# Kernel tuning notes

Measured on AMD Instinct MI355X. Metric: run time of the kernel, lower is better.

Reference implementation:

```python
import jax, jax.numpy as jnp
import numpy as np

N = 10000      # nodes
E = 160000     # edges
F_IN = 128     # input_dim
HID = 128      # hidden_dim = per-head channels (concat=False)
OUT = 128      # output_dim
H = 4          # heads
L = 4          # layers (all 128->128 here, so params stack)


def setup_inputs() -> dict:
    key = jax.random.key(0)
    ks = jax.random.split(key, 12)
    x = jax.random.normal(ks[0], (N, F_IN), dtype=jnp.float32)
    edge_index = jax.random.randint(ks[1], (2, E), 0, N, dtype=jnp.int64)
    s = 1.0 / np.sqrt(F_IN)
    Wq = jax.random.normal(ks[2], (L, F_IN, H * HID), dtype=jnp.float32) * s
    bq = jnp.zeros((L, H * HID), dtype=jnp.float32)
    Wk = jax.random.normal(ks[3], (L, F_IN, H * HID), dtype=jnp.float32) * s
    bk = jnp.zeros((L, H * HID), dtype=jnp.float32)
    Wv = jax.random.normal(ks[4], (L, F_IN, H * HID), dtype=jnp.float32) * s
    bv = jnp.zeros((L, H * HID), dtype=jnp.float32)
    Wskip = jax.random.normal(ks[5], (L, F_IN, HID), dtype=jnp.float32) * s
    bskip = jnp.zeros((L, HID), dtype=jnp.float32)
    return {"x": x, "edge_index": edge_index, "Wq": Wq, "bq": bq,
            "Wk": Wk, "bk": bk, "Wv": Wv, "bv": bv,
            "Wskip": Wskip, "bskip": bskip}


def _transformer_conv(x, src, dst, Wq, bq, Wk, bk, Wv, bv, Ws, bs):
    # PyG TransformerConv, concat=False (mean over heads), root_weight=True
    n = x.shape[0]
    q = (x @ Wq + bq).reshape(n, H, HID)
    k = (x @ Wk + bk).reshape(n, H, HID)
    v = (x @ Wv + bv).reshape(n, H, HID)
    # per-edge attention logits: [E, H]
    alpha = jnp.einsum('ehc,ehc->eh', q[dst], k[src]) / jnp.sqrt(jnp.float32(HID))
    # segment softmax over destination node
    m = jax.ops.segment_max(alpha, dst, num_segments=n)          # [N, H]
    e = jnp.exp(alpha - m[dst])                                  # [E, H]
    z = jax.ops.segment_sum(e, dst, num_segments=n)              # [N, H]
    a = e / z[dst]                                               # [E, H]
    msg = a[:, :, None] * v[src]                                 # [E, H, C]
    out = jax.ops.segment_sum(msg, dst, num_segments=n)          # [N, H, C]
    out = out.mean(axis=1)                                       # concat=False
    return out + x @ Ws + bs                                     # skip (root_weight)


def reference(x, edge_index, Wq, bq, Wk, bk, Wv, bv, Wskip, bskip):
    src = edge_index[0]
    dst = edge_index[1]
    h = x
    for l in range(L - 1):
        h = _transformer_conv(h, src, dst, Wq[l], bq[l], Wk[l], bk[l],
                              Wv[l], bv[l], Wskip[l], bskip[l])
        h = jax.nn.relu(h)  # dropout p in eval/reference is identity
    h = _transformer_conv(h, src, dst, Wq[-1], bq[-1], Wk[-1], bk[-1],
                          Wv[-1], bv[-1], Wskip[-1], bskip[-1])
    return h
```

## Files before the change

### kernel.cpp

```cpp
#include <hip/hip_runtime.h>
#include <math.h>

static constexpr int F  = 128;
static constexpr int H  = 4;
static constexpr int HF = 512;
static constexpr int NCP = 640;
static constexpr int LAYERS = 4;

typedef __attribute__((ext_vector_type(8))) short bf16x8;
typedef __attribute__((ext_vector_type(4))) float f32x4;

__device__ __forceinline__ unsigned short f2bf(float f) {
    union { float f; unsigned u; } v; v.f = f;
    unsigned r = (v.u + 0x7FFFu + ((v.u >> 16) & 1u)) >> 16;
    return (unsigned short)r;
}
__device__ __forceinline__ float bf2f(unsigned short b) {
    union { unsigned u; float f; } v; v.u = ((unsigned)b) << 16;
    return v.f;
}

__device__ __forceinline__ float row16_sum(float x) {
    int t;
    t = __builtin_amdgcn_update_dpp(0, __float_as_int(x), 0xB1, 0xF, 0xF, true);
    x += __int_as_float(t);
    t = __builtin_amdgcn_update_dpp(0, __float_as_int(x), 0x4E, 0xF, 0xF, true);
    x += __int_as_float(t);
    t = __builtin_amdgcn_update_dpp(0, __float_as_int(x), 0x124, 0xF, 0xF, true);
    x += __int_as_float(t);
    t = __builtin_amdgcn_update_dpp(0, __float_as_int(x), 0x128, 0xF, 0xF, true);
    x += __int_as_float(t);
    return x;
}

__global__ void hist_kernel(const int* __restrict__ dst, int* __restrict__ deg, int E) {
    int e = blockIdx.x * blockDim.x + threadIdx.x;
    if (e < E) atomicAdd(&deg[dst[e]], 1);
}

__global__ void scan_kernel(const int* __restrict__ deg, int* __restrict__ row_ptr, int n) {
    __shared__ int wsum[16];
    __shared__ int carry_s, wtot_s;
    const int tid = threadIdx.x;
    const int lane = tid & 63;
    const int wid = tid >> 6;
    if (tid == 0) { carry_s = 0; row_ptr[0] = 0; }
    __syncthreads();
    for (int base = 0; base < n; base += 1024) {
        int i = base + tid;
        int x = (i < n) ? deg[i] : 0;
#pragma unroll
        for (int off = 1; off < 64; off <<= 1) {
            int t = __shfl_up(x, off, 64);
            if (lane >= off) x += t;
        }
        if (lane == 63) wsum[wid] = x;
        __syncthreads();
        if (tid == 0) {
            int s = 0;
#pragma unroll
            for (int j = 0; j < 16; ++j) { int t = wsum[j]; wsum[j] = s; s += t; }
            wtot_s = s;
        }
        __syncthreads();
        int incl = x + wsum[wid] + carry_s;
        if (i < n) row_ptr[i + 1] = incl;
        __syncthreads();
        if (tid == 0) carry_s += wtot_s;
        __syncthreads();
    }
}

__global__ void scatter_kernel(const int* __restrict__ src, const int* __restrict__ dst,
                               const int* __restrict__ row_ptr, int* __restrict__ cursor,
                               int* __restrict__ csr_src, int E) {
    int e = blockIdx.x * blockDim.x + threadIdx.x;
    if (e < E) {
        int d = dst[e];
        int pos = atomicAdd(&cursor[d], 1);
        csr_src[row_ptr[d] + pos] = src[e];
    }
}

static constexpr int NB_CONV  = 1250;
static constexpr int NB_WQK   = 64;
static constexpr int NB_WS    = 64;
static constexpr int NB_BPOST = 256;
static constexpr int NB_BIAS  = LAYERS;
static constexpr int NB_PREP  = NB_CONV + NB_WQK + NB_WS + NB_BPOST + NB_BIAS;

__global__ __launch_bounds__(256) void prep_kernel(
    const float* __restrict__ x, unsigned short* __restrict__ h_bf, int n4,
    const float* __restrict__ Wq, const float* __restrict__ Wk,
    const float* __restrict__ Wv, const float* __restrict__ Ws,
    const float* __restrict__ bq, const float* __restrict__ bs, const float* __restrict__ bv,
    unsigned short* __restrict__ Bpre, unsigned short* __restrict__ Bpost,
    float* __restrict__ biasPre, float* __restrict__ biasPost, float scale)
{
    __shared__ __attribute__((aligned(16))) float smem[64 * 33 * 2];
    const int tid = threadIdx.x;
    int b = blockIdx.x;

    if (b < NB_CONV) {
        int i = b * 256 + tid;
        if (i < n4) {
            float4 v = *(const float4*)(x + (size_t)i * 4);
            ushort4 o;
            o.x = f2bf(v.x); o.y = f2bf(v.y); o.z = f2bf(v.z); o.w = f2bf(v.w);
            *(ushort4*)(h_bf + (size_t)i * 4) = o;
        }
        return;
    }
    b -= NB_CONV;
    if (b < NB_WQK) {
        float (*As)[33] = (float (*)[33])smem;
        float (*Bs)[33] = (float (*)[33])(smem + 64 * 33);
        const int bx = b & 1, by = (b >> 1) & 1, lh = b >> 2;
        const int l = lh >> 2, h = lh & 3;
        const int c0 = by * 64, k0 = bx * 64;
        const float* Ab = Wk + (size_t)l * 65536 + h * 128;
        const float* Bb = Wq + (size_t)l * 65536 + h * 128;
        const int tx = tid & 15, ty = tid >> 4;
        float acc[4][4] = {};
        for (int jj = 0; jj < 128; jj += 32) {
#pragma unroll
            for (int rep = 0; rep < 2; ++rep) {
                int f = tid + rep * 256;
                int r = f >> 3, j4 = (f & 7) * 4;
                float4 a = *(const float4*)(Ab + (size_t)(c0 + r) * 512 + jj + j4);
                As[r][j4 + 0] = a.x; As[r][j4 + 1] = a.y; As[r][j4 + 2] = a.z; As[r][j4 + 3] = a.w;
                float4 bb = *(const float4*)(Bb + (size_t)(k0 + r) * 512 + jj + j4);
                Bs[r][j4 + 0] = bb.x; Bs[r][j4 + 1] = bb.y; Bs[r][j4 + 2] = bb.z; Bs[r][j4 + 3] = bb.w;
            }
            __syncthreads();
#pragma unroll
            for (int j = 0; j < 32; ++j) {
                float a0 = As[ty * 4 + 0][j], a1 = As[ty * 4 + 1][j];
                float a2 = As[ty * 4 + 2][j], a3 = As[ty * 4 + 3][j];
                float b0 = Bs[tx * 4 + 0][j], b1 = Bs[tx * 4 + 1][j];
                float b2 = Bs[tx * 4 + 2][j], b3 = Bs[tx * 4 + 3][j];
                acc[0][0] += a0 * b0; acc[0][1] += a0 * b1; acc[0][2] += a0 * b2; acc[0][3] += a0 * b3;
                acc[1][0] += a1 * b0; acc[1][1] += a1 * b1; acc[1][2] += a1 * b2; acc[1][3] += a1 * b3;
                acc[2][0] += a2 * b0; acc[2][1] += a2 * b1; acc[2][2] += a2 * b2; acc[2][3] += a2 * b3;
                acc[3][0] += a3 * b0; acc[3][1] += a3 * b1; acc[3][2] += a3 * b2; acc[3][3] += a3 * b3;
            }
            __syncthreads();
        }
#pragma unroll
        for (int i = 0; i < 4; ++i)
#pragma unroll
            for (int t = 0; t < 4; ++t) {
                int c = c0 + ty * 4 + i;
                int k = k0 + tx * 4 + t;
                Bpre[(size_t)l * NCP * 128 + (size_t)(h * 128 + c) * 128 + k] = f2bf(scale * acc[i][t]);
            }
        return;
    }
    b -= NB_WQK;
    if (b < NB_WS) {
        unsigned short (*t)[33] = (unsigned short (*)[33])smem;
        const int bx = b & 3, by = (b >> 2) & 3, l = b >> 4;
        const int k0 = bx * 32, n0 = by * 32;
        const int cx = tid & 31, ry = tid >> 5;
#pragma unroll
        for (int rr = 0; rr < 32; rr += 8) {
            int k = k0 + ry + rr;
            t[ry + rr][cx] = f2bf(Ws[(size_t)l * 16384 + (size_t)k * 128 + n0 + cx]);
        }
        __syncthreads();
#pragma unroll
        for (int rr = 0; rr < 32; rr += 8) {
            int n = n0 + ry + rr;
            Bpre[(size_t)l * NCP * 128 + (size_t)(512 + n) * 128 + k0 + cx] = t[cx][ry + rr];
        }
        return;
    }
    b -= NB_WS;
    if (b < NB_BPOST) {
        unsigned short (*t)[33] = (unsigned short (*)[33])smem;
        const int bx = b & 3, by = (b >> 2) & 3, lh = b >> 4;
        const int l = lh >> 2, h = lh & 3;
        const int ci0 = bx * 32, co0 = by * 32;
        const int cx = tid & 31, ry = tid >> 5;
#pragma unroll
        for (int rr = 0; rr < 32; rr += 8) {
            int ci = ci0 + ry + rr;
            t[ry + rr][cx] = f2bf(0.25f * Wv[(size_t)l * 65536 + (size_t)ci * 512 + h * 128 + co0 + cx]);
        }
        __syncthreads();
#pragma unroll
        for (int rr = 0; rr < 32; rr += 8) {
            int co = co0 + ry + rr;
            Bpost[(size_t)l * 65536 + (size_t)co * 512 + h * 128 + ci0 + cx] = t[cx][ry + rr];
        }
        return;
    }
    b -= NB_BPOST;
    {
        const int l = b;
        for (int n = tid; n < 512; n += 256) {
            int h = n >> 7, c = n & 127;
            float s = 0.f;
            for (int j = 0; j < 128; ++j)
                s += bq[(size_t)l * 512 + h * 128 + j] * Wk[(size_t)l * 65536 + (size_t)c * 512 + h * 128 + j];
            biasPre[(size_t)l * NCP + n] = s * scale;
        }
        for (int c = tid; c < 128; c += 256) {
            float s = 0.f;
            for (int h = 0; h < 4; ++h) s += bv[(size_t)l * 512 + h * 128 + c];
            biasPost[(size_t)l * 128 + c] = 0.25f * s + bs[(size_t)l * 128 + c];
        }
    }
}

__global__ __launch_bounds__(256) void gemm_pre(
    const unsigned short* __restrict__ Abf,
    const unsigned short* __restrict__ Bt,
    const float* __restrict__ bias,
    unsigned short* __restrict__ Qt,
    int M)
{
    __shared__ unsigned short As[128][72];
    __shared__ unsigned short Bs[128][72];

    const int tid = threadIdx.x;
    const int wave = tid >> 6, lane = tid & 63;
    const int lane16 = lane & 15, quad = lane >> 4;
    const int wr = wave >> 1, wc = wave & 1;
    const int row0 = blockIdx.y * 128;
    const int col0 = blockIdx.x * 128;

    f32x4 acc[4][4] = {};

    for (int kk = 0; kk < 128; kk += 64) {
#pragma unroll
        for (int j = 0; j < 4; ++j) {
            int c = tid + j * 256;
            int r = c >> 3, c8 = (c & 7) * 8;
            bf16x8 v = {};
            if (row0 + r < M) v = *(const bf16x8*)(Abf + (size_t)(row0 + r) * 128 + kk + c8);
            *(bf16x8*)&As[r][c8] = v;
        }
#pragma unroll
        for (int j = 0; j < 4; ++j) {
            int c = tid + j * 256;
            int r = c >> 3, c8 = (c & 7) * 8;
            *(bf16x8*)&Bs[r][c8] = *(const bf16x8*)(Bt + (size_t)(col0 + r) * 128 + kk + c8);
        }
        __syncthreads();

#pragma unroll
        for (int ks = 0; ks < 2; ++ks) {
            bf16x8 a[4], b[4];
#pragma unroll
            for (int i = 0; i < 4; ++i)
                a[i] = *(const bf16x8*)&As[wr * 64 + i * 16 + lane16][ks * 32 + quad * 8];
#pragma unroll
            for (int i = 0; i < 4; ++i)
                b[i] = *(const bf16x8*)&Bs[wc * 64 + i * 16 + lane16][ks * 32 + quad * 8];
#pragma unroll
            for (int mi = 0; mi < 4; ++mi)
#pragma unroll
                for (int ni = 0; ni < 4; ++ni)
                    acc[mi][ni] = __builtin_amdgcn_mfma_f32_16x16x32_bf16(
                        a[mi], b[ni], acc[mi][ni], 0, 0, 0);
        }
        __syncthreads();
    }

#pragma unroll
    for (int mi = 0; mi < 4; ++mi) {
        int rowb = row0 + wr * 64 + mi * 16 + quad * 4;
#pragma unroll
        for (int ni = 0; ni < 4; ++ni) {
            int col = col0 + wc * 64 + ni * 16 + lane16;
            float bv = bias[col];
#pragma unroll
            for (int r = 0; r < 4; ++r) {
                int gr = rowb + r;
                if (gr < M) Qt[(size_t)gr * 512 + col] = f2bf(acc[mi][ni][r] + bv);
            }
        }
    }
}

__global__ __launch_bounds__(128, 4) void attn_agg(
    const unsigned short* __restrict__ Qt,
    const unsigned short* __restrict__ Hb,
    const int* __restrict__ row_ptr,
    const int* __restrict__ csr_src,
    unsigned short* __restrict__ Agg,
    int N)
{
    __shared__ float part[4][16][10];

    const int tid = threadIdx.x;
    const int wv  = tid >> 6;
    const int g   = (tid >> 4) & 3;
    const int l16 = tid & 15;
    const int node = blockIdx.x;

    const float NEG = -3e38f;

    float qf[8];
    {
        bf16x8 qv = *(const bf16x8*)(Qt + (size_t)node * HF + g * F + l16 * 8);
#pragma unroll
        for (int j = 0; j < 8; ++j) qf[j] = bf2f((unsigned short)qv[j]);
    }
    const unsigned short* Hl = Hb + (size_t)l16 * 8;

    const int beg = row_ptr[node];
    const int end = row_ptr[node + 1];

    float m = NEG, z = 0.f;
    float acc[8];
#pragma unroll
    for (int j = 0; j < 8; ++j) acc[j] = 0.f;

    const int begw = beg + wv * 4;
    if (begw < end) {
        const int last = end - 1;
        const int NB = (end - begw + 7) >> 3;

#define CLD(i) csr_src[(i) < last ? (i) : last]

        int a0 = CLD(begw + 0), a1 = CLD(begw + 1), a2 = CLD(begw + 2), a3 = CLD(begw + 3);
        bf16x8 hA0 = *(const bf16x8*)(Hl + (size_t)a0 * F);
        bf16x8 hA1 = *(const bf16x8*)(Hl + (size_t)a1 * F);
        bf16x8 hA2 = *(const bf16x8*)(Hl + (size_t)a2 * F);
        bf16x8 hA3 = *(const bf16x8*)(Hl + (size_t)a3 * F);
        int b0 = CLD(begw + 8), b1 = CLD(begw + 9), b2 = CLD(begw + 10), b3 = CLD(begw + 11);
        bf16x8 hB0 = *(const bf16x8*)(Hl + (size_t)b0 * F);
        bf16x8 hB1 = *(const bf16x8*)(Hl + (size_t)b1 * F);
        bf16x8 hB2 = *(const bf16x8*)(Hl + (size_t)b2 * F);
        bf16x8 hB3 = *(const bf16x8*)(Hl + (size_t)b3 * F);
        a0 = CLD(begw + 16); a1 = CLD(begw + 17); a2 = CLD(begw + 18); a3 = CLD(begw + 19);
        b0 = CLD(begw + 24); b1 = CLD(begw + 25); b2 = CLD(begw + 26); b3 = CLD(begw + 27);
        __builtin_amdgcn_sched_barrier(0);

#define ATTN_BATCH(H0, H1, H2, H3, I0, I1, I2, I3)                              \
    {                                                                           \
        float hf[4][8];                                                         \
        _Pragma("unroll")                                                       \
        for (int j = 0; j < 8; ++j) {                                           \
            hf[0][j] = bf2f((unsigned short)H0[j]);                             \
            hf[1][j] = bf2f((unsigned short)H1[j]);                             \
            hf[2][j] = bf2f((unsigned short)H2[j]);                             \
            hf[3][j] = bf2f((unsigned short)H3[j]);                             \
        }                                                                       \
        if (k + 2 < NB) {                                                       \
            H0 = *(const bf16x8*)(Hl + (size_t)I0 * F);                         \
            H1 = *(const bf16x8*)(Hl + (size_t)I1 * F);                         \
            H2 = *(const bf16x8*)(Hl + (size_t)I2 * F);                         \
            H3 = *(const bf16x8*)(Hl + (size_t)I3 * F);                         \
            I0 = CLD(base + 32); I1 = CLD(base + 33);                           \
            I2 = CLD(base + 34); I3 = CLD(base + 35);                           \
        }                                                                       \
        __builtin_amdgcn_sched_barrier(0);   \
        float p0 = 0.f, p1 = 0.f, p2 = 0.f, p3 = 0.f;                           \
        _Pragma("unroll")                                                       \
        for (int j = 0; j < 8; ++j) {                                           \
            p0 += qf[j] * hf[0][j]; p1 += qf[j] * hf[1][j];                     \
            p2 += qf[j] * hf[2][j]; p3 += qf[j] * hf[3][j];                     \
        }                                                                       \
        p0 = row16_sum(p0); p1 = row16_sum(p1);                                 \
        p2 = row16_sum(p2); p3 = row16_sum(p3);                                 \
        const int nv = end - base;                                              \
        if (nv < 4) { if (nv < 2) p1 = NEG; if (nv < 3) p2 = NEG; p3 = NEG; }   \
        float bm = fmaxf(fmaxf(p0, p1), fmaxf(p2, p3));                         \
        float mn = fmaxf(m, bm);                                                \
        float rs = exp2f(m - mn);                                               \
        float w0 = exp2f(p0 - mn), w1 = exp2f(p1 - mn);                         \
        float w2 = exp2f(p2 - mn), w3 = exp2f(p3 - mn);                         \
        z = z * rs + (w0 + w1) + (w2 + w3);                                     \
        _Pragma("unroll")                                                       \
        for (int j = 0; j < 8; ++j)                                             \
            acc[j] = acc[j] * rs + w0 * hf[0][j] + w1 * hf[1][j]                \
                   + w2 * hf[2][j] + w3 * hf[3][j];                             \
        m = mn;                                                                 \
    }

        int base = begw;
        int k = 0;
        for (;;) {
            ATTN_BATCH(hA0, hA1, hA2, hA3, a0, a1, a2, a3)
            ++k; base += 8;
            if (k >= NB) break;
            ATTN_BATCH(hB0, hB1, hB2, hB3, b0, b1, b2, b3)
            ++k; base += 8;
            if (k >= NB) break;
        }
#undef ATTN_BATCH
#undef CLD
    }

    if (wv == 1) {
#pragma unroll
        for (int j = 0; j < 8; ++j) part[g][l16][j] = acc[j];
        part[g][l16][8] = m;
        part[g][l16][9] = z;
    }
    __syncthreads();
    if (wv == 0) {
        float om = part[g][l16][8];
        float oz = part[g][l16][9];
        float M  = fmaxf(m, om);
        float sa = exp2f(m - M);
        float sb = exp2f(om - M);
        float zz = z * sa + oz * sb;
        float inv = (zz > 0.f) ? 1.f / zz : 0.f;
        bf16x8 o;
#pragma unroll
        for (int j = 0; j < 8; ++j)
            o[j] = (short)f2bf((acc[j] * sa + part[g][l16][j] * sb) * inv);
        *(bf16x8*)(Agg + (size_t)node * HF + g * F + l16 * 8) = o;
    }
}

__global__ __launch_bounds__(256) void gemm_post(
    const unsigned short* __restrict__ Agg,
    const unsigned short* __restrict__ Hc,
    const unsigned short* __restrict__ Bt,
    const unsigned short* __restrict__ Bsk,
    const float* __restrict__ bias,
    float* __restrict__ out_f,
    unsigned short* __restrict__ out_bf,
    int relu, int M)
{
    __shared__ unsigned short As[64][72];
    __shared__ unsigned short Bs[64][72];

    const int tid = threadIdx.x;
    const int wave = tid >> 6, lane = tid & 63;
    const int lane16 = lane & 15, quad = lane >> 4;
    const int row0 = blockIdx.y * 64;
    const int col0 = blockIdx.x * 64;

    f32x4 acc[4] = {};

    for (int kk = 0; kk < 640; kk += 64) {
        const bool sk = kk >= 512;
        const int k0 = sk ? kk - 512 : kk;
#pragma unroll
        for (int rep = 0; rep < 2; ++rep) {
            int c = tid + rep * 256;
            int r = c >> 3, c8 = (c & 7) * 8;
            bf16x8 v = {};
            if (row0 + r < M)
                v = sk ? *(const bf16x8*)(Hc  + (size_t)(row0 + r) * 128 + k0 + c8)
                       : *(const bf16x8*)(Agg + (size_t)(row0 + r) * 512 + k0 + c8);
            *(bf16x8*)&As[r][c8] = v;
            *(bf16x8*)&Bs[r][c8] = sk
                ? *(const bf16x8*)(Bsk + (size_t)(col0 + r) * 128 + k0 + c8)
                : *(const bf16x8*)(Bt  + (size_t)(col0 + r) * 512 + k0 + c8);
        }
        __syncthreads();

#pragma unroll
        for (int ks = 0; ks < 2; ++ks) {
            bf16x8 b = *(const bf16x8*)&Bs[wave * 16 + lane16][ks * 32 + quad * 8];
#pragma unroll
            for (int mt = 0; mt < 4; ++mt) {
                bf16x8 a = *(const bf16x8*)&As[mt * 16 + lane16][ks * 32 + quad * 8];
                acc[mt] = __builtin_amdgcn_mfma_f32_16x16x32_bf16(a, b, acc[mt], 0, 0, 0);
            }
        }
        __syncthreads();
    }

    const int col = col0 + wave * 16 + lane16;
    const float bcol = bias[col];
#pragma unroll
    for (int mt = 0; mt < 4; ++mt) {
#pragma unroll
        for (int r = 0; r < 4; ++r) {
            int row = row0 + mt * 16 + quad * 4 + r;
            if (row < M) {
                float v = acc[mt][r] + bcol;
                if (relu) v = fmaxf(v, 0.f);
                if (out_f)  out_f[(size_t)row * 128 + col] = v;
                if (out_bf) out_bf[(size_t)row * 128 + col] = f2bf(v);
            }
        }
    }
}

extern "C" void kernel_launch(void* const* d_in, const int* in_sizes, int n_in,
                              void* d_out, int out_size, void* d_ws, size_t ws_size,
                              hipStream_t stream) {
    const float* x     = (const float*)d_in[0];
    const int*   ei    = (const int*)d_in[1];
    const float* Wq    = (const float*)d_in[2];
    const float* bq    = (const float*)d_in[3];
    const float* Wk    = (const float*)d_in[4];
    const float* bk    = (const float*)d_in[5];
    const float* Wv    = (const float*)d_in[6];
    const float* bv    = (const float*)d_in[7];
    const float* Wskip = (const float*)d_in[8];
    const float* bskip = (const float*)d_in[9];
    float* out = (float*)d_out;
    (void)bk;

    const int N = in_sizes[0] / F;
    const int E = in_sizes[1] / 2;
    const float scale = 0.08838834764831845f * 1.4426950408889634f;

    const int* src = ei;
    const int* dst = ei + E;

    char* p = (char*)d_ws;
    float* biasPreP = (float*)p;               p += (size_t)LAYERS * NCP * sizeof(float);
    float* biasPostP= (float*)p;               p += (size_t)LAYERS * 128 * sizeof(float);
    unsigned short* h0    = (unsigned short*)p; p += (size_t)N * F * sizeof(unsigned short);
    unsigned short* h1    = (unsigned short*)p; p += (size_t)N * F * sizeof(unsigned short);
    unsigned short* Qt    = (unsigned short*)p; p += (size_t)N * HF * sizeof(unsigned short);
    unsigned short* AggB  = (unsigned short*)p; p += (size_t)N * HF * sizeof(unsigned short);
    unsigned short* BpreP = (unsigned short*)p; p += (size_t)LAYERS * NCP * 128 * sizeof(unsigned short);
    unsigned short* BpostP= (unsigned short*)p; p += (size_t)LAYERS * 128 * 512 * sizeof(unsigned short);
    int* deg     = (int*)p;                    p += (size_t)N * sizeof(int);
    int* cursor  = (int*)p;                    p += (size_t)N * sizeof(int);
    int* row_ptr = (int*)p;                    p += (size_t)(N + 1) * sizeof(int);
    int* csr_src = (int*)p;

    hipMemsetAsync(deg, 0, 2 * (size_t)N * sizeof(int), stream);
    {
        int blocks = (E + 255) / 256;
        hist_kernel<<<blocks, 256, 0, stream>>>(dst, deg, E);
        scan_kernel<<<1, 1024, 0, stream>>>(deg, row_ptr, N);
        scatter_kernel<<<blocks, 256, 0, stream>>>(src, dst, row_ptr, cursor, csr_src, E);
    }

    prep_kernel<<<NB_PREP, 256, 0, stream>>>(x, h0, N * F / 4,
                                             Wq, Wk, Wv, Wskip,
                                             bq, bskip, bv,
                                             BpreP, BpostP, biasPreP, biasPostP, scale);

    const int rowBlocks128 = (N + 127) / 128;
    const int rowBlocks64  = (N + 63) / 64;

    unsigned short* hcur = h0;
    unsigned short* hnxt = h1;
    for (int l = 0; l < LAYERS; ++l) {
        dim3 gridPre(4, rowBlocks128);
        gemm_pre<<<gridPre, 256, 0, stream>>>(hcur,
                                              BpreP + (size_t)l * NCP * 128,
                                              biasPreP + (size_t)l * NCP,
                                              Qt, N);

        attn_agg<<<N, 128, 0, stream>>>(Qt, hcur, row_ptr, csr_src, AggB, N);

        float* out_f = nullptr;
        unsigned short* out_bf = nullptr;
        int relu;
        if (l == LAYERS - 1) { out_f = out; relu = 0; }
        else { out_bf = hnxt; relu = 1; }

        dim3 gridPost(2, rowBlocks64);
        gemm_post<<<gridPost, 256, 0, stream>>>(AggB, hcur,
                                                BpostP + (size_t)l * 128 * 512,
                                                BpreP + (size_t)l * NCP * 128 + (size_t)512 * 128,
                                                biasPostP + (size_t)l * 128,
                                                out_f, out_bf, relu, N);

        unsigned short* t = hcur; hcur = hnxt; hnxt = t;
    }
}
```

Measured before the change: 254.1 us.

## Fuse all layer stages into one persistent cooperative kernel with grid syncs

```diff
diff --git a/kernel.cpp b/kernel.cpp
--- a/kernel.cpp
+++ b/kernel.cpp
@@ -1,5 +1,8 @@
 #include <hip/hip_runtime.h>
+#include <hip/hip_cooperative_groups.h>
 #include <math.h>
+
+namespace cg = cooperative_groups;
 
 static constexpr int F  = 128;
 static constexpr int H  = 4;
@@ -213,131 +216,137 @@
     }
 }
 
-__global__ __launch_bounds__(256) void gemm_pre(
-    const unsigned short* __restrict__ Abf,
-    const unsigned short* __restrict__ Bt,
-    const float* __restrict__ bias,
-    unsigned short* __restrict__ Qt,
-    int M)
+__global__ __launch_bounds__(256) void layers_kernel(
+    unsigned short* __restrict__ h0, unsigned short* __restrict__ h1,
+    unsigned short* __restrict__ Qt, unsigned short* __restrict__ Agg,
+    const unsigned short* __restrict__ Bpre, const unsigned short* __restrict__ Bpost,
+    const float* __restrict__ biasPre, const float* __restrict__ biasPost,
+    const int* __restrict__ row_ptr, const int* __restrict__ csr_src,
+    float* __restrict__ out, int N)
 {
-    __shared__ unsigned short As[128][72];
-    __shared__ unsigned short Bs[128][72];
+    cg::grid_group grid = cg::this_grid();
+    __shared__ __attribute__((aligned(16))) char smem[36864];
 
     const int tid = threadIdx.x;
-    const int wave = tid >> 6, lane = tid & 63;
-    const int lane16 = lane & 15, quad = lane >> 4;
-    const int wr = wave >> 1, wc = wave & 1;
-    const int row0 = blockIdx.y * 128;
-    const int col0 = blockIdx.x * 128;
-
-    f32x4 acc[4][4] = {};
-
-    for (int kk = 0; kk < 128; kk += 64) {
-#pragma unroll
-        for (int j = 0; j < 4; ++j) {
-            int c = tid + j * 256;
-            int r = c >> 3, c8 = (c & 7) * 8;
-            bf16x8 v = {};
-            if (row0 + r < M) v = *(const bf16x8*)(Abf + (size_t)(row0 + r) * 128 + kk + c8);
-            *(bf16x8*)&As[r][c8] = v;
-        }
-#pragma unroll
-        for (int j = 0; j < 4; ++j) {
-            int c = tid + j * 256;
-            int r = c >> 3, c8 = (c & 7) * 8;
-            *(bf16x8*)&Bs[r][c8] = *(const bf16x8*)(Bt + (size_t)(col0 + r) * 128 + kk + c8);
-        }
-        __syncthreads();
-
-#pragma unroll
-        for (int ks = 0; ks < 2; ++ks) {
-            bf16x8 a[4], b[4];
-#pragma unroll
-            for (int i = 0; i < 4; ++i)
-                a[i] = *(const bf16x8*)&As[wr * 64 + i * 16 + lane16][ks * 32 + quad * 8];
-#pragma unroll
-            for (int i = 0; i < 4; ++i)
-                b[i] = *(const bf16x8*)&Bs[wc * 64 + i * 16 + lane16][ks * 32 + quad * 8];
-#pragma unroll
-            for (int mi = 0; mi < 4; ++mi)
-#pragma unroll
-                for (int ni = 0; ni < 4; ++ni)
-                    acc[mi][ni] = __builtin_amdgcn_mfma_f32_16x16x32_bf16(
-                        a[mi], b[ni], acc[mi][ni], 0, 0, 0);
-        }
-        __syncthreads();
-    }
-
-#pragma unroll
-    for (int mi = 0; mi < 4; ++mi) {
-        int rowb = row0 + wr * 64 + mi * 16 + quad * 4;
-#pragma unroll
-        for (int ni = 0; ni < 4; ++ni) {
-            int col = col0 + wc * 64 + ni * 16 + lane16;
-            float bv = bias[col];
-#pragma unroll
-            for (int r = 0; r < 4; ++r) {
-                int gr = rowb + r;
-                if (gr < M) Qt[(size_t)gr * 512 + col] = f2bf(acc[mi][ni][r] + bv);
+    const int rb128 = (N + 127) >> 7;
+    const int rb64  = (N + 63) >> 6;
+    const float NEG = -3e38f;
+
+    unsigned short* hcur = h0;
+    unsigned short* hnxt = h1;
+
+    for (int l = 0; l < LAYERS; ++l) {
+        const unsigned short* BtPre = Bpre + (size_t)l * NCP * 128;
+        const float* bPre = biasPre + (size_t)l * NCP;
+
+        {
+            unsigned short (*As)[72] = (unsigned short (*)[72])smem;
+            unsigned short (*Bs)[72] = (unsigned short (*)[72])(smem + 128 * 72 * 2);
+            const int wave = tid >> 6, lane = tid & 63;
+            const int lane16 = lane & 15, quad = lane >> 4;
+            const int wr = wave >> 1, wc = wave & 1;
+            const int nT = 4 * rb128;
+            for (int tile = blockIdx.x; tile < nT; tile += gridDim.x) {
+                const int row0 = (tile >> 2) * 128;
+                const int col0 = (tile & 3) * 128;
+                f32x4 acc[4][4] = {};
+                for (int kk = 0; kk < 128; kk += 64) {
+#pragma unroll
+                    for (int j = 0; j < 4; ++j) {
+                        int c = tid + j * 256;
+                        int r = c >> 3, c8 = (c & 7) * 8;
+                        bf16x8 v = {};
+                        if (row0 + r < N) v = *(const bf16x8*)(hcur + (size_t)(row0 + r) * 128 + kk + c8);
+                        *(bf16x8*)&As[r][c8] = v;
+                    }
+#pragma unroll
+                    for (int j = 0; j < 4; ++j) {
+                        int c = tid + j * 256;
+                        int r = c >> 3, c8 = (c & 7) * 8;
+                        *(bf16x8*)&Bs[r][c8] = *(const bf16x8*)(BtPre + (size_t)(col0 + r) * 128 + kk + c8);
+                    }
+                    __syncthreads();
+#pragma unroll
+                    for (int ks = 0; ks < 2; ++ks) {
+                        bf16x8 a[4], b[4];
+#pragma unroll
+                        for (int i = 0; i < 4; ++i)
+                            a[i] = *(const bf16x8*)&As[wr * 64 + i * 16 + lane16][ks * 32 + quad * 8];
+#pragma unroll
+                        for (int i = 0; i < 4; ++i)
+                            b[i] = *(const bf16x8*)&Bs[wc * 64 + i * 16 + lane16][ks * 32 + quad * 8];
+#pragma unroll
+                        for (int mi = 0; mi < 4; ++mi)
+#pragma unroll
+                            for (int ni = 0; ni < 4; ++ni)
+                                acc[mi][ni] = __builtin_amdgcn_mfma_f32_16x16x32_bf16(
+                                    a[mi], b[ni], acc[mi][ni], 0, 0, 0);
+                    }
+                    __syncthreads();
+                }
+#pragma unroll
+                for (int mi = 0; mi < 4; ++mi) {
+                    int rowb = row0 + wr * 64 + mi * 16 + quad * 4;
+#pragma unroll
+                    for (int ni = 0; ni < 4; ++ni) {
+                        int col = col0 + wc * 64 + ni * 16 + lane16;
+                        float bv = bPre[col];
+#pragma unroll
+                        for (int r = 0; r < 4; ++r) {
+                            int gr = rowb + r;
+                            if (gr < N) Qt[(size_t)gr * 512 + col] = f2bf(acc[mi][ni][r] + bv);
+                        }
+                    }
+                }
             }
         }
-    }
-}
-
-__global__ __launch_bounds__(128, 4) void attn_agg(
-    const unsigned short* __restrict__ Qt,
-    const unsigned short* __restrict__ Hb,
-    const int* __restrict__ row_ptr,
-    const int* __restrict__ csr_src,
-    unsigned short* __restrict__ Agg,
-    int N)
-{
-    __shared__ float part[4][16][10];
-
-    const int tid = threadIdx.x;
-    const int wv  = tid >> 6;
-    const int g   = (tid >> 4) & 3;
-    const int l16 = tid & 15;
-    const int node = blockIdx.x;
-
-    const float NEG = -3e38f;
-
-    float qf[8];
-    {
-        bf16x8 qv = *(const bf16x8*)(Qt + (size_t)node * HF + g * F + l16 * 8);
-#pragma unroll
-        for (int j = 0; j < 8; ++j) qf[j] = bf2f((unsigned short)qv[j]);
-    }
-    const unsigned short* Hl = Hb + (size_t)l16 * 8;
-
-    const int beg = row_ptr[node];
-    const int end = row_ptr[node + 1];
-
-    float m = NEG, z = 0.f;
-    float acc[8];
-#pragma unroll
-    for (int j = 0; j < 8; ++j) acc[j] = 0.f;
-
-    const int begw = beg + wv * 4;
-    if (begw < end) {
-        const int last = end - 1;
-        const int NB = (end - begw + 7) >> 3;
+        grid.sync();
+
+        {
+            float (*part)[16][10] = (float (*)[16][10])smem;
+            const int half = tid >> 7;
+            const int wv  = (tid >> 6) & 1;
+            const int g   = (tid >> 4) & 3;
+            const int l16 = tid & 15;
+            const unsigned short* Hl = hcur + (size_t)l16 * 8;
+
+            for (int nb = blockIdx.x * 2; nb < N; nb += gridDim.x * 2) {
+                const int node = nb + half;
+                const bool valid = node < N;
+
+                float m = NEG, z = 0.f;
+                float acc[8];
+#pragma unroll
+                for (int j = 0; j < 8; ++j) acc[j] = 0.f;
+
+                if (valid) {
+                    float qf[8];
+                    {
+                        bf16x8 qv = *(const bf16x8*)(Qt + (size_t)node * HF + g * F + l16 * 8);
+#pragma unroll
+                        for (int j = 0; j < 8; ++j) qf[j] = bf2f((unsigned short)qv[j]);
+                    }
+                    const int beg = row_ptr[node];
+                    const int end = row_ptr[node + 1];
+                    const int begw = beg + wv * 4;
+                    if (begw < end) {
+                        const int last = end - 1;
+                        const int NB = (end - begw + 7) >> 3;
 
 #define CLD(i) csr_src[(i) < last ? (i) : last]
-
-        int a0 = CLD(begw + 0), a1 = CLD(begw + 1), a2 = CLD(begw + 2), a3 = CLD(begw + 3);
-        bf16x8 hA0 = *(const bf16x8*)(Hl + (size_t)a0 * F);
-        bf16x8 hA1 = *(const bf16x8*)(Hl + (size_t)a1 * F);
-        bf16x8 hA2 = *(const bf16x8*)(Hl + (size_t)a2 * F);
-        bf16x8 hA3 = *(const bf16x8*)(Hl + (size_t)a3 * F);
-        int b0 = CLD(begw + 8), b1 = CLD(begw + 9), b2 = CLD(begw + 10), b3 = CLD(begw + 11);
-        bf16x8 hB0 = *(const bf16x8*)(Hl + (size_t)b0 * F);
-        bf16x8 hB1 = *(const bf16x8*)(Hl + (size_t)b1 * F);
-        bf16x8 hB2 = *(const bf16x8*)(Hl + (size_t)b2 * F);
-        bf16x8 hB3 = *(const bf16x8*)(Hl + (size_t)b3 * F);
-        a0 = CLD(begw + 16); a1 = CLD(begw + 17); a2 = CLD(begw + 18); a3 = CLD(begw + 19);
-        b0 = CLD(begw + 24); b1 = CLD(begw + 25); b2 = CLD(begw + 26); b3 = CLD(begw + 27);
-        __builtin_amdgcn_sched_barrier(0);
+                        int a0 = CLD(begw + 0), a1 = CLD(begw + 1), a2 = CLD(begw + 2), a3 = CLD(begw + 3);
+                        bf16x8 hA0 = *(const bf16x8*)(Hl + (size_t)a0 * F);
+                        bf16x8 hA1 = *(const bf16x8*)(Hl + (size_t)a1 * F);
+                        bf16x8 hA2 = *(const bf16x8*)(Hl + (size_t)a2 * F);
+                        bf16x8 hA3 = *(const bf16x8*)(Hl + (size_t)a3 * F);
+                        int b0 = CLD(begw + 8), b1 = CLD(begw + 9), b2 = CLD(begw + 10), b3 = CLD(begw + 11);
+                        bf16x8 hB0 = *(const bf16x8*)(Hl + (size_t)b0 * F);
+                        bf16x8 hB1 = *(const bf16x8*)(Hl + (size_t)b1 * F);
+                        bf16x8 hB2 = *(const bf16x8*)(Hl + (size_t)b2 * F);
+                        bf16x8 hB3 = *(const bf16x8*)(Hl + (size_t)b3 * F);
+                        a0 = CLD(begw + 16); a1 = CLD(begw + 17); a2 = CLD(begw + 18); a3 = CLD(begw + 19);
+                        b0 = CLD(begw + 24); b1 = CLD(begw + 25); b2 = CLD(begw + 26); b3 = CLD(begw + 27);
+                        __builtin_amdgcn_sched_barrier(0);
 
 #define ATTN_BATCH(H0, H1, H2, H3, I0, I1, I2, I3)                              \
     {                                                                           \
@@ -357,7 +366,7 @@
             I0 = CLD(base + 32); I1 = CLD(base + 33);                           \
             I2 = CLD(base + 34); I3 = CLD(base + 35);                           \
         }                                                                       \
-        __builtin_amdgcn_sched_barrier(0);   \
+        __builtin_amdgcn_sched_barrier(0);                                      \
         float p0 = 0.f, p1 = 0.f, p2 = 0.f, p3 = 0.f;                           \
         _Pragma("unroll")                                                       \
         for (int j = 0; j < 8; ++j) {                                           \
@@ -381,6 +390,262 @@
         m = mn;                                                                 \
     }
 
+                        int base = begw;
+                        int k = 0;
+                        for (;;) {
+                            ATTN_BATCH(hA0, hA1, hA2, hA3, a0, a1, a2, a3)
+                            ++k; base += 8;
+                            if (k >= NB) break;
+                            ATTN_BATCH(hB0, hB1, hB2, hB3, b0, b1, b2, b3)
+                            ++k; base += 8;
+                            if (k >= NB) break;
+                        }
+#undef ATTN_BATCH
+#undef CLD
+                    }
+                }
+                __syncthreads();
+                if (valid && wv == 1) {
+#pragma unroll
+                    for (int j = 0; j < 8; ++j) part[(half << 2) + g][l16][j] = acc[j];
+                    part[(half << 2) + g][l16][8] = m;
+                    part[(half << 2) + g][l16][9] = z;
+                }
+                __syncthreads();
+                if (valid && wv == 0) {
+                    float om = part[(half << 2) + g][l16][8];
+                    float oz = part[(half << 2) + g][l16][9];
+                    float M  = fmaxf(m, om);
+                    float sa = exp2f(m - M);
+                    float sb = exp2f(om - M);
+                    float zz = z * sa + oz * sb;
+                    float inv = (zz > 0.f) ? 1.f / zz : 0.f;
+                    bf16x8 o;
+#pragma unroll
+                    for (int j = 0; j < 8; ++j)
+                        o[j] = (short)f2bf((acc[j] * sa + part[(half << 2) + g][l16][j] * sb) * inv);
+                    *(bf16x8*)(Agg + (size_t)node * HF + g * F + l16 * 8) = o;
+                }
+                __syncthreads();
+            }
+        }
+        grid.sync();
+
+        {
+            const unsigned short* BtPost = Bpost + (size_t)l * 128 * 512;
+            const unsigned short* Bsk = Bpre + (size_t)l * NCP * 128 + (size_t)512 * 128;
+            const float* bPost = biasPost + (size_t)l * 128;
+            float* out_f = (l == LAYERS - 1) ? out : nullptr;
+            unsigned short* out_bf = (l == LAYERS - 1) ? nullptr : hnxt;
+            const int relu = (l == LAYERS - 1) ? 0 : 1;
+
+            unsigned short (*As)[72] = (unsigned short (*)[72])smem;
+            unsigned short (*Bs)[72] = (unsigned short (*)[72])(smem + 64 * 72 * 2);
+            const int wave = tid >> 6, lane = tid & 63;
+            const int lane16 = lane & 15, quad = lane >> 4;
+            const int nT = 2 * rb64;
+            for (int tile = blockIdx.x; tile < nT; tile += gridDim.x) {
+                const int row0 = (tile >> 1) * 64;
+                const int col0 = (tile & 1) * 64;
+                f32x4 acc[4] = {};
+                for (int kk = 0; kk < 640; kk += 64) {
+                    const bool sk = kk >= 512;
+                    const int k0 = sk ? kk - 512 : kk;
+#pragma unroll
+                    for (int rep = 0; rep < 2; ++rep) {
+                        int c = tid + rep * 256;
+                        int r = c >> 3, c8 = (c & 7) * 8;
+                        bf16x8 v = {};
+                        if (row0 + r < N)
+                            v = sk ? *(const bf16x8*)(hcur + (size_t)(row0 + r) * 128 + k0 + c8)
+                                   : *(const bf16x8*)(Agg  + (size_t)(row0 + r) * 512 + k0 + c8);
+                        *(bf16x8*)&As[r][c8] = v;
+                        *(bf16x8*)&Bs[r][c8] = sk
+                            ? *(const bf16x8*)(Bsk    + (size_t)(col0 + r) * 128 + k0 + c8)
+                            : *(const bf16x8*)(BtPost + (size_t)(col0 + r) * 512 + k0 + c8);
+                    }
+                    __syncthreads();
+#pragma unroll
+                    for (int ks = 0; ks < 2; ++ks) {
+                        bf16x8 b = *(const bf16x8*)&Bs[wave * 16 + lane16][ks * 32 + quad * 8];
+#pragma unroll
+                        for (int mt = 0; mt < 4; ++mt) {
+                            bf16x8 a = *(const bf16x8*)&As[mt * 16 + lane16][ks * 32 + quad * 8];
+                            acc[mt] = __builtin_amdgcn_mfma_f32_16x16x32_bf16(a, b, acc[mt], 0, 0, 0);
+                        }
+                    }
+                    __syncthreads();
+                }
+                const int col = col0 + wave * 16 + lane16;
+                const float bcol = bPost[col];
+#pragma unroll
+                for (int mt = 0; mt < 4; ++mt) {
+#pragma unroll
+                    for (int r = 0; r < 4; ++r) {
+                        int row = row0 + mt * 16 + quad * 4 + r;
+                        if (row < N) {
+                            float v = acc[mt][r] + bcol;
+                            if (relu) v = fmaxf(v, 0.f);
+                            if (out_f)  out_f[(size_t)row * 128 + col] = v;
+                            if (out_bf) out_bf[(size_t)row * 128 + col] = f2bf(v);
+                        }
+                    }
+                }
+            }
+        }
+        grid.sync();
+
+        unsigned short* t = hcur; hcur = hnxt; hnxt = t;
+    }
+}
+
+__global__ __launch_bounds__(256) void gemm_pre(
+    const unsigned short* __restrict__ Abf, const unsigned short* __restrict__ Bt,
+    const float* __restrict__ bias, unsigned short* __restrict__ Qt, int M)
+{
+    __shared__ unsigned short As[128][72];
+    __shared__ unsigned short Bs[128][72];
+    const int tid = threadIdx.x;
+    const int wave = tid >> 6, lane = tid & 63;
+    const int lane16 = lane & 15, quad = lane >> 4;
+    const int wr = wave >> 1, wc = wave & 1;
+    const int row0 = blockIdx.y * 128;
+    const int col0 = blockIdx.x * 128;
+    f32x4 acc[4][4] = {};
+    for (int kk = 0; kk < 128; kk += 64) {
+#pragma unroll
+        for (int j = 0; j < 4; ++j) {
+            int c = tid + j * 256;
+            int r = c >> 3, c8 = (c & 7) * 8;
+            bf16x8 v = {};
+            if (row0 + r < M) v = *(const bf16x8*)(Abf + (size_t)(row0 + r) * 128 + kk + c8);
+            *(bf16x8*)&As[r][c8] = v;
+        }
+#pragma unroll
+        for (int j = 0; j < 4; ++j) {
+            int c = tid + j * 256;
+            int r = c >> 3, c8 = (c & 7) * 8;
+            *(bf16x8*)&Bs[r][c8] = *(const bf16x8*)(Bt + (size_t)(col0 + r) * 128 + kk + c8);
+        }
+        __syncthreads();
+#pragma unroll
+        for (int ks = 0; ks < 2; ++ks) {
+            bf16x8 a[4], b[4];
+#pragma unroll
+            for (int i = 0; i < 4; ++i)
+                a[i] = *(const bf16x8*)&As[wr * 64 + i * 16 + lane16][ks * 32 + quad * 8];
+#pragma unroll
+            for (int i = 0; i < 4; ++i)
+                b[i] = *(const bf16x8*)&Bs[wc * 64 + i * 16 + lane16][ks * 32 + quad * 8];
+#pragma unroll
+            for (int mi = 0; mi < 4; ++mi)
+#pragma unroll
+                for (int ni = 0; ni < 4; ++ni)
+                    acc[mi][ni] = __builtin_amdgcn_mfma_f32_16x16x32_bf16(
+                        a[mi], b[ni], acc[mi][ni], 0, 0, 0);
+        }
+        __syncthreads();
+    }
+#pragma unroll
+    for (int mi = 0; mi < 4; ++mi) {
+        int rowb = row0 + wr * 64 + mi * 16 + quad * 4;
+#pragma unroll
+        for (int ni = 0; ni < 4; ++ni) {
+            int col = col0 + wc * 64 + ni * 16 + lane16;
+            float bv = bias[col];
+#pragma unroll
+            for (int r = 0; r < 4; ++r) {
+                int gr = rowb + r;
+                if (gr < M) Qt[(size_t)gr * 512 + col] = f2bf(acc[mi][ni][r] + bv);
+            }
+        }
+    }
+}
+
+__global__ __launch_bounds__(128, 4) void attn_agg(
+    const unsigned short* __restrict__ Qt, const unsigned short* __restrict__ Hb,
+    const int* __restrict__ row_ptr, const int* __restrict__ csr_src,
+    unsigned short* __restrict__ Agg, int N)
+{
+    __shared__ float part[4][16][10];
+    const int tid = threadIdx.x;
+    const int wv  = tid >> 6;
+    const int g   = (tid >> 4) & 3;
+    const int l16 = tid & 15;
+    const int node = blockIdx.x;
+    const float NEG = -3e38f;
+    float qf[8];
+    {
+        bf16x8 qv = *(const bf16x8*)(Qt + (size_t)node * HF + g * F + l16 * 8);
+#pragma unroll
+        for (int j = 0; j < 8; ++j) qf[j] = bf2f((unsigned short)qv[j]);
+    }
+    const unsigned short* Hl = Hb + (size_t)l16 * 8;
+    const int beg = row_ptr[node];
+    const int end = row_ptr[node + 1];
+    float m = NEG, z = 0.f;
+    float acc[8];
+#pragma unroll
+    for (int j = 0; j < 8; ++j) acc[j] = 0.f;
+    const int begw = beg + wv * 4;
+    if (begw < end) {
+        const int last = end - 1;
+        const int NB = (end - begw + 7) >> 3;
+#define CLD(i) csr_src[(i) < last ? (i) : last]
+        int a0 = CLD(begw + 0), a1 = CLD(begw + 1), a2 = CLD(begw + 2), a3 = CLD(begw + 3);
+        bf16x8 hA0 = *(const bf16x8*)(Hl + (size_t)a0 * F);
+        bf16x8 hA1 = *(const bf16x8*)(Hl + (size_t)a1 * F);
+        bf16x8 hA2 = *(const bf16x8*)(Hl + (size_t)a2 * F);
+        bf16x8 hA3 = *(const bf16x8*)(Hl + (size_t)a3 * F);
+        int b0 = CLD(begw + 8), b1 = CLD(begw + 9), b2 = CLD(begw + 10), b3 = CLD(begw + 11);
+        bf16x8 hB0 = *(const bf16x8*)(Hl + (size_t)b0 * F);
+        bf16x8 hB1 = *(const bf16x8*)(Hl + (size_t)b1 * F);
+        bf16x8 hB2 = *(const bf16x8*)(Hl + (size_t)b2 * F);
+        bf16x8 hB3 = *(const bf16x8*)(Hl + (size_t)b3 * F);
+        a0 = CLD(begw + 16); a1 = CLD(begw + 17); a2 = CLD(begw + 18); a3 = CLD(begw + 19);
+        b0 = CLD(begw + 24); b1 = CLD(begw + 25); b2 = CLD(begw + 26); b3 = CLD(begw + 27);
+        __builtin_amdgcn_sched_barrier(0);
+#define ATTN_BATCH(H0, H1, H2, H3, I0, I1, I2, I3)                              \
+    {                                                                           \
+        float hf[4][8];                                                         \
+        _Pragma("unroll")                                                       \
+        for (int j = 0; j < 8; ++j) {                                           \
+            hf[0][j] = bf2f((unsigned short)H0[j]);                             \
+            hf[1][j] = bf2f((unsigned short)H1[j]);                             \
+            hf[2][j] = bf2f((unsigned short)H2[j]);                             \
+            hf[3][j] = bf2f((unsigned short)H3[j]);                             \
+        }                                                                       \
+        if (k + 2 < NB) {                                                       \
+            H0 = *(const bf16x8*)(Hl + (size_t)I0 * F);                         \
+            H1 = *(const bf16x8*)(Hl + (size_t)I1 * F);                         \
+            H2 = *(const bf16x8*)(Hl + (size_t)I2 * F);                         \
+            H3 = *(const bf16x8*)(Hl + (size_t)I3 * F);                         \
+            I0 = CLD(base + 32); I1 = CLD(base + 33);                           \
+            I2 = CLD(base + 34); I3 = CLD(base + 35);                           \
+        }                                                                       \
+        __builtin_amdgcn_sched_barrier(0);                                      \
+        float p0 = 0.f, p1 = 0.f, p2 = 0.f, p3 = 0.f;                           \
+        _Pragma("unroll")                                                       \
+        for (int j = 0; j < 8; ++j) {                                           \
+            p0 += qf[j] * hf[0][j]; p1 += qf[j] * hf[1][j];                     \
+            p2 += qf[j] * hf[2][j]; p3 += qf[j] * hf[3][j];                     \
+        }                                                                       \
+        p0 = row16_sum(p0); p1 = row16_sum(p1);                                 \
+        p2 = row16_sum(p2); p3 = row16_sum(p3);                                 \
+        const int nv = end - base;                                              \
+        if (nv < 4) { if (nv < 2) p1 = NEG; if (nv < 3) p2 = NEG; p3 = NEG; }   \
+        float bm = fmaxf(fmaxf(p0, p1), fmaxf(p2, p3));                         \
+        float mn = fmaxf(m, bm);                                                \
+        float rs = exp2f(m - mn);                                               \
+        float w0 = exp2f(p0 - mn), w1 = exp2f(p1 - mn);                         \
+        float w2 = exp2f(p2 - mn), w3 = exp2f(p3 - mn);                         \
+        z = z * rs + (w0 + w1) + (w2 + w3);                                     \
+        _Pragma("unroll")                                                       \
+        for (int j = 0; j < 8; ++j)                                             \
+            acc[j] = acc[j] * rs + w0 * hf[0][j] + w1 * hf[1][j]                \
+                   + w2 * hf[2][j] + w3 * hf[3][j];                             \
+        m = mn;                                                                 \
+    }
         int base = begw;
         int k = 0;
         for (;;) {
@@ -394,7 +659,6 @@
 #undef ATTN_BATCH
 #undef CLD
     }
-
     if (wv == 1) {
 #pragma unroll
         for (int j = 0; j < 8; ++j) part[g][l16][j] = acc[j];
@@ -419,26 +683,19 @@
 }
 
 __global__ __launch_bounds__(256) void gemm_post(
-    const unsigned short* __restrict__ Agg,
-    const unsigned short* __restrict__ Hc,
-    const unsigned short* __restrict__ Bt,
-    const unsigned short* __restrict__ Bsk,
-    const float* __restrict__ bias,
-    float* __restrict__ out_f,
-    unsigned short* __restrict__ out_bf,
-    int relu, int M)
+    const unsigned short* __restrict__ Agg, const unsigned short* __restrict__ Hc,
+    const unsigned short* __restrict__ Bt, const unsigned short* __restrict__ Bsk,
+    const float* __restrict__ bias, float* __restrict__ out_f,
+    unsigned short* __restrict__ out_bf, int relu, int M)
 {
     __shared__ unsigned short As[64][72];
     __shared__ unsigned short Bs[64][72];
-
     const int tid = threadIdx.x;
     const int wave = tid >> 6, lane = tid & 63;
     const int lane16 = lane & 15, quad = lane >> 4;
     const int row0 = blockIdx.y * 64;
     const int col0 = blockIdx.x * 64;
-
     f32x4 acc[4] = {};
-
     for (int kk = 0; kk < 640; kk += 64) {
         const bool sk = kk >= 512;
         const int k0 = sk ? kk - 512 : kk;
@@ -456,7 +713,6 @@
                 : *(const bf16x8*)(Bt  + (size_t)(col0 + r) * 512 + k0 + c8);
         }
         __syncthreads();
-
 #pragma unroll
         for (int ks = 0; ks < 2; ++ks) {
             bf16x8 b = *(const bf16x8*)&Bs[wave * 16 + lane16][ks * 32 + quad * 8];
@@ -468,7 +724,6 @@
         }
         __syncthreads();
     }
-
     const int col = col0 + wave * 16 + lane16;
     const float bcol = bias[col];
 #pragma unroll
@@ -536,33 +791,49 @@
                                              bq, bskip, bv,
                                              BpreP, BpostP, biasPreP, biasPostP, scale);
 
-    const int rowBlocks128 = (N + 127) / 128;
-    const int rowBlocks64  = (N + 63) / 64;
-
-    unsigned short* hcur = h0;
-    unsigned short* hnxt = h1;
-    for (int l = 0; l < LAYERS; ++l) {
-        dim3 gridPre(4, rowBlocks128);
-        gemm_pre<<<gridPre, 256, 0, stream>>>(hcur,
-                                              BpreP + (size_t)l * NCP * 128,
-                                              biasPreP + (size_t)l * NCP,
-                                              Qt, N);
-
-        attn_agg<<<N, 128, 0, stream>>>(Qt, hcur, row_ptr, csr_src, AggB, N);
-
-        float* out_f = nullptr;
-        unsigned short* out_bf = nullptr;
-        int relu;
-        if (l == LAYERS - 1) { out_f = out; relu = 0; }
-        else { out_bf = hnxt; relu = 1; }
-
-        dim3 gridPost(2, rowBlocks64);
-        gemm_post<<<gridPost, 256, 0, stream>>>(AggB, hcur,
-                                                BpostP + (size_t)l * 128 * 512,
-                                                BpreP + (size_t)l * NCP * 128 + (size_t)512 * 128,
-                                                biasPostP + (size_t)l * 128,
-                                                out_f, out_bf, relu, N);
-
-        unsigned short* t = hcur; hcur = hnxt; hnxt = t;
-    }
-}
+    int maxPerCU = 0;
+    hipOccupancyMaxActiveBlocksPerMultiprocessor(&maxPerCU,
+        reinterpret_cast<const void*>(layers_kernel), 256, 0);
+    if (maxPerCU < 1) maxPerCU = 1;
+    int nB = maxPerCU * 256;
+    if (nB > 512) nB = 512;
+
+    int Nv = N;
+    void* kargs[] = { (void*)&h0, (void*)&h1, (void*)&Qt, (void*)&AggB,
+                      (void*)&BpreP, (void*)&BpostP, (void*)&biasPreP, (void*)&biasPostP,
+                      (void*)&row_ptr, (void*)&csr_src, (void*)&out, (void*)&Nv };
+    hipError_t cerr = hipLaunchCooperativeKernel(
+        reinterpret_cast<const void*>(layers_kernel),
+        dim3(nB), dim3(256), kargs, 0, stream);
+
+    if (cerr != hipSuccess) {
+        const int rowBlocks128 = (N + 127) / 128;
+        const int rowBlocks64  = (N + 63) / 64;
+        unsigned short* hcur = h0;
+        unsigned short* hnxt = h1;
+        for (int l = 0; l < LAYERS; ++l) {
+            dim3 gridPre(4, rowBlocks128);
+            gemm_pre<<<gridPre, 256, 0, stream>>>(hcur,
+                                                  BpreP + (size_t)l * NCP * 128,
+                                                  biasPreP + (size_t)l * NCP,
+                                                  Qt, N);
+
+            attn_agg<<<N, 128, 0, stream>>>(Qt, hcur, row_ptr, csr_src, AggB, N);
+
+            float* out_f = nullptr;
+            unsigned short* out_bf = nullptr;
+            int relu;
+            if (l == LAYERS - 1) { out_f = out; relu = 0; }
+            else { out_bf = hnxt; relu = 1; }
+
+            dim3 gridPost(2, rowBlocks64);
+            gemm_post<<<gridPost, 256, 0, stream>>>(AggB, hcur,
+                                                    BpostP + (size_t)l * 128 * 512,
+                                                    BpreP + (size_t)l * NCP * 128 + (size_t)512 * 128,
+                                                    biasPostP + (size_t)l * 128,
+                                                    out_f, out_bf, relu, N);
+
+            unsigned short* t = hcur; hcur = hnxt; hnxt = t;
+        }
+    }
+}
```

Result: slower. 785.4 us (+209.2%).
